# Performance work log

Measured on AMD Instinct MI355X. Metric: run time of the kernel, lower is better.

The kernel has to match this reference:

```python
import jax, jax.numpy as jnp
import numpy as np

N_ENT = 100000


def setup_inputs() -> dict:
    key = jax.random.key(0)
    ks = jax.random.split(key, 10)
    B, D, O, R, E = 50000, 128, 128, 8, 200000
    return {
        "embeddings": jax.random.normal(ks[0], (N_ENT, D), dtype=jnp.float32),
        "head_e": jax.random.normal(ks[1], (B, D), dtype=jnp.float32),
        "tail_e": jax.random.normal(ks[2], (B, D), dtype=jnp.float32),
        "relation_kernel": jax.random.normal(ks[3], (R, D, O), dtype=jnp.float32),
        "self_kernel": jax.random.normal(ks[4], (D, O), dtype=jnp.float32),
        "edge_val": jax.random.uniform(ks[5], (R, E), dtype=jnp.float32),
        "head_idx": jax.random.randint(ks[6], (B,), 0, N_ENT, dtype=jnp.int32),
        "tail_idx": jax.random.randint(ks[7], (B,), 0, N_ENT, dtype=jnp.int32),
        "edge_src": jax.random.randint(ks[8], (R, E), 0, N_ENT, dtype=jnp.int32),
        "edge_dst": jax.random.randint(ks[9], (R, E), 0, N_ENT, dtype=jnp.int32),
    }


def reference(embeddings, head_e, tail_e, relation_kernel, self_kernel,
              edge_val, head_idx, tail_idx, edge_src, edge_dst):
    # Per-relation SpMM: sum_emb[r, row] = sum_{edges e of r with src=row} val[e] * embeddings[dst[e]]
    def spmm(src, dst, val):
        return jax.ops.segment_sum(embeddings[dst] * val[:, None], src,
                                   num_segments=embeddings.shape[0])
    sum_emb = jax.vmap(spmm)(edge_src, edge_dst, edge_val)  # [R, N, D]

    head_update = jnp.take(sum_emb, head_idx, axis=1)  # [R, B, D]
    tail_update = jnp.take(sum_emb, tail_idx, axis=1)  # [R, B, D]

    head_output = head_e @ self_kernel + jnp.einsum('rbd,rdo->bo', head_update, relation_kernel)
    tail_output = tail_e @ self_kernel + jnp.einsum('rbd,rdo->bo', tail_update, relation_kernel)
    return (jax.nn.sigmoid(head_output), jax.nn.sigmoid(tail_output))
```

## Files before the change

### kernel.cpp

```cpp
#include <hip/hip_runtime.h>
#include <hip/hip_bf16.h>
#include <math.h>

#define N_ENT 100000
#define NB    50000
#define NE    200000
#define RR    8
#define NETOT (RR * NE)
#define NSEG  (RR * N_ENT)

typedef float f32x4  __attribute__((ext_vector_type(4)));
typedef short s16x8  __attribute__((ext_vector_type(8)));

__device__ __forceinline__ void split2(float x, short& h, short& l)
{
    unsigned uh = __float_as_uint(x) & 0xffff0000u;
    h = (short)(uh >> 16);
    float r = x - __uint_as_float(uh);
    l = (short)(__float_as_uint(r) >> 16);
}

__global__ __launch_bounds__(256)
void ktconv_k(const float* __restrict__ rel_k, const float* __restrict__ self_k,
              short* __restrict__ Kth, short* __restrict__ Ktl)
{
    const int r = blockIdx.x;
    const float* src = (r < 8) ? rel_k + (size_t)r * 16384 : self_k;
    short* oh = Kth + (size_t)r * 16384;
    short* ol = Ktl + (size_t)r * 16384;
    for (int i = 0; i < 64; ++i) {
        int ix = i * 256 + threadIdx.x;
        int d = ix >> 7, o = ix & 127;
        short h, l;
        split2(src[ix], h, l);
        oh[o * 128 + d] = h;
        ol[o * 128 + d] = l;
    }
}

template<bool FINAL, bool ACCUM>
__global__ __launch_bounds__(256)
void gemm_mfma_k(const float* __restrict__ X, int xstride,
                 const short* __restrict__ Kth, const short* __restrict__ Ktl,
                 int nkc,
                 const float* __restrict__ Abuf, const int* __restrict__ idx,
                 float* __restrict__ out, int nrows)
{
    __shared__ short Bh[128][136];
    __shared__ short Bl[128][136];

    const int t     = threadIdx.x;
    const int wv    = t >> 6;
    const int lane  = t & 63;
    const int col16 = lane & 15;
    const int g     = lane >> 4;
    const int rowbase = blockIdx.x * 128 + wv * 32;

    f32x4 acc[2][8];
#pragma unroll
    for (int m = 0; m < 2; ++m)
#pragma unroll
        for (int c = 0; c < 8; ++c) acc[m][c] = (f32x4){0.f, 0.f, 0.f, 0.f};

    for (int kc = 0; kc < nkc; ++kc) {
        __syncthreads();
        {
            const s16x8* gh = (const s16x8*)(Kth + (size_t)kc * 16384);
            const s16x8* gl = (const s16x8*)(Ktl + (size_t)kc * 16384);
#pragma unroll
            for (int i = 0; i < 8; ++i) {
                int f = t + i * 256;
                int o = f >> 4, c = f & 15;
                *(s16x8*)&Bh[o][c * 8] = gh[f];
                *(s16x8*)&Bl[o][c * 8] = gl[f];
            }
        }
        __syncthreads();

#pragma unroll
        for (int s = 0; s < 4; ++s) {
            s16x8 ah[2], al[2];
#pragma unroll
            for (int m = 0; m < 2; ++m) {
                int r = rowbase + m * 16 + col16;
                if (r > nrows - 1) r = nrows - 1;
                const float* xp = X + (size_t)r * xstride + kc * 128 + s * 32 + g * 8;
                float4 u0 = *(const float4*)xp;
                float4 u1 = *(const float4*)(xp + 4);
                float u[8] = {u0.x, u0.y, u0.z, u0.w, u1.x, u1.y, u1.z, u1.w};
#pragma unroll
                for (int j = 0; j < 8; ++j) {
                    short h, l; split2(u[j], h, l);
                    ah[m][j] = h; al[m][j] = l;
                }
            }
#pragma unroll
            for (int c = 0; c < 8; ++c) {
                s16x8 bh = *(const s16x8*)&Bh[c * 16 + col16][s * 32 + g * 8];
                s16x8 bl = *(const s16x8*)&Bl[c * 16 + col16][s * 32 + g * 8];
#pragma unroll
                for (int m = 0; m < 2; ++m) {
                    acc[m][c] = __builtin_amdgcn_mfma_f32_16x16x32_bf16(ah[m], bh, acc[m][c], 0, 0, 0);
                    acc[m][c] = __builtin_amdgcn_mfma_f32_16x16x32_bf16(ah[m], bl, acc[m][c], 0, 0, 0);
                    acc[m][c] = __builtin_amdgcn_mfma_f32_16x16x32_bf16(al[m], bh, acc[m][c], 0, 0, 0);
                }
            }
        }
    }

#pragma unroll
    for (int m = 0; m < 2; ++m) {
#pragma unroll
        for (int j = 0; j < 4; ++j) {
            int row = rowbase + m * 16 + g * 4 + j;
            if (row >= nrows) continue;
            float* op = out + (size_t)row * 128;
            if (FINAL) {
                int gi = idx[row];
                const float* Ar = Abuf + (size_t)gi * 128;
#pragma unroll
                for (int c = 0; c < 8; ++c) {
                    int col = c * 16 + col16;
                    float x = acc[m][c][j] + Ar[col];
                    op[col] = 1.f / (1.f + __expf(-x));
                }
            } else if (ACCUM) {
#pragma unroll
                for (int c = 0; c < 8; ++c) {
                    int col = c * 16 + col16;
                    op[col] += acc[m][c][j];
                }
            } else {
#pragma unroll
                for (int c = 0; c < 8; ++c)
                    op[c * 16 + col16] = acc[m][c][j];
            }
        }
    }
}

__global__ __launch_bounds__(256)
void count_k(const int* __restrict__ edge_src, unsigned* __restrict__ cnt)
{
    int g = blockIdx.x * 256 + threadIdx.x;
    int r = g / NE;
    int src = edge_src[g];
    atomicAdd(&cnt[r * N_ENT + src], 1u);
}

__global__ __launch_bounds__(256)
void scan1_k(const unsigned* __restrict__ cnt, unsigned* __restrict__ offs,
             unsigned* __restrict__ bsum)
{
    __shared__ unsigned s[256];
    const int t = threadIdx.x;
    const int base = blockIdx.x * 1024;
    unsigned v[4], sum = 0;
#pragma unroll
    for (int i = 0; i < 4; ++i) {
        int ix = base + t * 4 + i;
        v[i] = (ix < NSEG) ? cnt[ix] : 0u;
        sum += v[i];
    }
    s[t] = sum; __syncthreads();
    for (int off = 1; off < 256; off <<= 1) {
        unsigned x = (t >= off) ? s[t - off] : 0u;
        __syncthreads();
        s[t] += x;
        __syncthreads();
    }
    unsigned run = s[t] - sum;
#pragma unroll
    for (int i = 0; i < 4; ++i) {
        int ix = base + t * 4 + i;
        if (ix < NSEG) offs[ix] = run;
        run += v[i];
    }
    if (t == 255) bsum[blockIdx.x] = s[255];
}

__global__ __launch_bounds__(256)
void scan2_k(unsigned* __restrict__ bsum, int nb)
{
    __shared__ unsigned s[256];
    __shared__ unsigned carry;
    const int t = threadIdx.x;
    if (t == 0) carry = 0;
    __syncthreads();
    for (int base = 0; base < nb; base += 256) {
        unsigned v = (base + t < nb) ? bsum[base + t] : 0u;
        s[t] = v; __syncthreads();
        for (int off = 1; off < 256; off <<= 1) {
            unsigned x = (t >= off) ? s[t - off] : 0u;
            __syncthreads();
            s[t] += x;
            __syncthreads();
        }
        unsigned tot = s[255];
        unsigned excl = s[t] - v + carry;
        if (base + t < nb) bsum[base + t] = excl;
        __syncthreads();
        if (t == 0) carry += tot;
        __syncthreads();
    }
}

__global__ __launch_bounds__(256)
void scan3_k(unsigned* __restrict__ offs, const unsigned* __restrict__ bsum)
{
    const int base = blockIdx.x * 1024;
    unsigned add = bsum[blockIdx.x];
#pragma unroll
    for (int i = 0; i < 4; ++i) {
        int ix = base + threadIdx.x * 4 + i;
        if (ix < NSEG) offs[ix] += add;
    }
    if (blockIdx.x == 0 && threadIdx.x == 0) offs[NSEG] = NETOT;
}

__global__ __launch_bounds__(256)
void fill_k(const int* __restrict__ edge_src, const int* __restrict__ edge_dst,
            const float* __restrict__ edge_val,
            const unsigned* __restrict__ offs, unsigned* __restrict__ cursor,
            int2* __restrict__ recs)
{
    int g = blockIdx.x * 256 + threadIdx.x;
    int r = g / NE;
    int src = edge_src[g];
    int seg = r * N_ENT + src;
    unsigned pos = offs[seg] + atomicAdd(&cursor[seg], 1u);
    int2 rec;
    rec.x = edge_dst[g];
    rec.y = __float_as_int(edge_val[g]);
    recs[pos] = rec;
}

__global__ __launch_bounds__(256)
void segsum_k(const unsigned* __restrict__ offs_r, const int2* __restrict__ recs,
              const float* __restrict__ emb, float* __restrict__ B, int nrel)
{
    int wid  = (blockIdx.x * 256 + threadIdx.x) >> 6;
    int lane = threadIdx.x & 63;
    int j = wid / N_ENT;
    int s = wid - j * N_ENT;
    unsigned e0 = offs_r[wid];
    unsigned e1 = offs_r[wid + 1];
    float2 acc = {0.f, 0.f};
    for (unsigned e = e0; e < e1; ++e) {
        int2 rec = recs[e];
        float v = __int_as_float(rec.y);
        float2 y = *(const float2*)(emb + (size_t)rec.x * 128 + lane * 2);
        acc.x = fmaf(v, y.x, acc.x);
        acc.y = fmaf(v, y.y, acc.y);
    }
    *(float2*)(B + ((size_t)s * nrel + j) * 128 + lane * 2) = acc;
}

extern "C" void kernel_launch(void* const* d_in, const int* in_sizes, int n_in,
                              void* d_out, int out_size, void* d_ws, size_t ws_size,
                              hipStream_t stream)
{
    const float* emb      = (const float*)d_in[0];
    const float* head_e   = (const float*)d_in[1];
    const float* tail_e   = (const float*)d_in[2];
    const float* rel_k    = (const float*)d_in[3];
    const float* self_k   = (const float*)d_in[4];
    const float* edge_val = (const float*)d_in[5];
    const int*   head_idx = (const int*)d_in[6];
    const int*   tail_idx = (const int*)d_in[7];
    const int*   edge_src = (const int*)d_in[8];
    const int*   edge_dst = (const int*)d_in[9];
    float* out = (float*)d_out;

    char* p = (char*)d_ws;
    auto take = [&](size_t bytes) -> char* {
        char* q = p; p += (bytes + 255) & ~(size_t)255; return q;
    };
    float*    A    = (float*)take((size_t)N_ENT * 128 * sizeof(float));
    int2*     recs = (int2*)take((size_t)NETOT * sizeof(int2));
    unsigned* cnt  = (unsigned*)take((size_t)NSEG * sizeof(unsigned));
    unsigned* offs = (unsigned*)take(((size_t)NSEG + 1) * sizeof(unsigned));
    unsigned* bsum = (unsigned*)take(1024 * sizeof(unsigned));
    short*    Kth  = (short*)take((size_t)9 * 16384 * sizeof(short));
    short*    Ktl  = (short*)take((size_t)9 * 16384 * sizeof(short));
    float*    Bbuf = (float*)p;

    size_t used    = (size_t)(p - (char*)d_ws);
    size_t avail   = (ws_size > used) ? ws_size - used : 0;
    size_t per_rel = (size_t)N_ENT * 128 * sizeof(float);
    int RPG = (int)(avail / per_rel);
    if (RPG > RR) RPG = RR;
    if (RPG < 1)  RPG = 1;

    const int NB1 = (NSEG + 1023) / 1024;
    dim3 blk(256);

    ktconv_k<<<9, blk, 0, stream>>>(rel_k, self_k, Kth, Ktl);
    hipMemsetAsync(cnt, 0, (size_t)NSEG * sizeof(unsigned), stream);
    count_k<<<NETOT / 256, blk, 0, stream>>>(edge_src, cnt);
    scan1_k<<<NB1, blk, 0, stream>>>(cnt, offs, bsum);
    scan2_k<<<1, blk, 0, stream>>>(bsum, NB1);
    scan3_k<<<NB1, blk, 0, stream>>>(offs, bsum);
    hipMemsetAsync(cnt, 0, (size_t)NSEG * sizeof(unsigned), stream);
    fill_k<<<NETOT / 256, blk, 0, stream>>>(edge_src, edge_dst, edge_val,
                                            offs, cnt, recs);

    const int gy = (N_ENT + 127) / 128;
    int first = 1;
    for (int g0 = 0; g0 < RR; ) {
        int nr = (RR - g0 < RPG) ? RR - g0 : RPG;
        int gs = nr * (N_ENT / 4);
        segsum_k<<<gs, blk, 0, stream>>>(offs + (size_t)g0 * N_ENT, recs,
                                         emb, Bbuf, nr);
        if (first)
            gemm_mfma_k<false, false><<<gy, blk, 0, stream>>>(
                Bbuf, nr * 128,
                Kth + (size_t)g0 * 16384, Ktl + (size_t)g0 * 16384, nr,
                nullptr, nullptr, A, N_ENT);
        else
            gemm_mfma_k<false, true><<<gy, blk, 0, stream>>>(
                Bbuf, nr * 128,
                Kth + (size_t)g0 * 16384, Ktl + (size_t)g0 * 16384, nr,
                nullptr, nullptr, A, N_ENT);
        first = 0;
        g0 += nr;
    }

    const int gb = (NB + 127) / 128;
    gemm_mfma_k<true, false><<<gb, blk, 0, stream>>>(
        head_e, 128, Kth + (size_t)8 * 16384, Ktl + (size_t)8 * 16384, 1,
        A, head_idx, out, NB);
    gemm_mfma_k<true, false><<<gb, blk, 0, stream>>>(
        tail_e, 128, Kth + (size_t)8 * 16384, Ktl + (size_t)8 * 16384, 1,
        A, tail_idx, out + (size_t)NB * 128, NB);
}
```

Baseline: 700.0 us.

## Batch segment-sum over relations per wave with prefetched edge gathers

```diff
diff --git a/kernel.cpp b/kernel.cpp
--- a/kernel.cpp
+++ b/kernel.cpp
@@ -235,25 +235,79 @@
     recs[pos] = rec;
 }
 
+template<int NR>
 __global__ __launch_bounds__(256)
 void segsum_k(const unsigned* __restrict__ offs_r, const int2* __restrict__ recs,
-              const float* __restrict__ emb, float* __restrict__ B, int nrel)
-{
-    int wid  = (blockIdx.x * 256 + threadIdx.x) >> 6;
-    int lane = threadIdx.x & 63;
-    int j = wid / N_ENT;
-    int s = wid - j * N_ENT;
-    unsigned e0 = offs_r[wid];
-    unsigned e1 = offs_r[wid + 1];
-    float2 acc = {0.f, 0.f};
-    for (unsigned e = e0; e < e1; ++e) {
-        int2 rec = recs[e];
-        float v = __int_as_float(rec.y);
-        float2 y = *(const float2*)(emb + (size_t)rec.x * 128 + lane * 2);
-        acc.x = fmaf(v, y.x, acc.x);
-        acc.y = fmaf(v, y.y, acc.y);
-    }
-    *(float2*)(B + ((size_t)s * nrel + j) * 128 + lane * 2) = acc;
+              const float* __restrict__ emb, float* __restrict__ B)
+{
+    constexpr int T = 4;
+    const int s    = (blockIdx.x * 256 + threadIdx.x) >> 6;
+    const int lane = threadIdx.x & 63;
+    if (s >= N_ENT) return;
+
+    unsigned e0[NR]; int n[NR];
+#pragma unroll
+    for (int j = 0; j < NR; ++j) {
+        unsigned a = offs_r[(size_t)j * N_ENT + s];
+        unsigned b = offs_r[(size_t)j * N_ENT + s + 1];
+        e0[j] = a; n[j] = (int)(b - a);
+    }
+
+    int2 rec[NR][T];
+#pragma unroll
+    for (int j = 0; j < NR; ++j)
+#pragma unroll
+        for (int i = 0; i < T; ++i)
+            if (i < n[j]) rec[j][i] = recs[e0[j] + i];
+
+    float2 y[NR][T];
+#pragma unroll
+    for (int j = 0; j < NR; ++j)
+#pragma unroll
+        for (int i = 0; i < T; ++i)
+            if (i < n[j])
+                y[j][i] = *(const float2*)(emb + (size_t)rec[j][i].x * 128 + lane * 2);
+
+    float2 acc[NR];
+#pragma unroll
+    for (int j = 0; j < NR; ++j) acc[j] = (float2){0.f, 0.f};
+#pragma unroll
+    for (int j = 0; j < NR; ++j)
+#pragma unroll
+        for (int i = 0; i < T; ++i)
+            if (i < n[j]) {
+                float v = __int_as_float(rec[j][i].y);
+                acc[j].x = fmaf(v, y[j][i].x, acc[j].x);
+                acc[j].y = fmaf(v, y[j][i].y, acc[j].y);
+            }
+
+#pragma unroll
+    for (int j = 0; j < NR; ++j) {
+        for (int i = T; i < n[j]; ++i) {
+            int2 rc = recs[e0[j] + i];
+            float v = __int_as_float(rc.y);
+            float2 yy = *(const float2*)(emb + (size_t)rc.x * 128 + lane * 2);
+            acc[j].x = fmaf(v, yy.x, acc[j].x);
+            acc[j].y = fmaf(v, yy.y, acc[j].y);
+        }
+    }
+
+#pragma unroll
+    for (int j = 0; j < NR; ++j)
+        *(float2*)(B + ((size_t)s * NR + j) * 128 + lane * 2) = acc[j];
+}
+
+static void launch_segsum(int nr, const unsigned* offs_r, const int2* recs,
+                          const float* emb, float* B, hipStream_t stream)
+{
+    dim3 blk(256);
+    const int blocks = (N_ENT * 64) / 256;
+    switch (nr) {
+    case 1: segsum_k<1><<<blocks, blk, 0, stream>>>(offs_r, recs, emb, B); break;
+    case 2: segsum_k<2><<<blocks, blk, 0, stream>>>(offs_r, recs, emb, B); break;
+    case 3: segsum_k<3><<<blocks, blk, 0, stream>>>(offs_r, recs, emb, B); break;
+    default: segsum_k<4><<<blocks, blk, 0, stream>>>(offs_r, recs, emb, B); break;
+    }
 }
 
 extern "C" void kernel_launch(void* const* d_in, const int* in_sizes, int n_in,
@@ -289,8 +343,8 @@
     size_t avail   = (ws_size > used) ? ws_size - used : 0;
     size_t per_rel = (size_t)N_ENT * 128 * sizeof(float);
     int RPG = (int)(avail / per_rel);
-    if (RPG > RR) RPG = RR;
-    if (RPG < 1)  RPG = 1;
+    if (RPG > 4) RPG = 4;
+    if (RPG < 1) RPG = 1;
 
     const int NB1 = (NSEG + 1023) / 1024;
     dim3 blk(256);
@@ -309,9 +363,7 @@
     int first = 1;
     for (int g0 = 0; g0 < RR; ) {
         int nr = (RR - g0 < RPG) ? RR - g0 : RPG;
-        int gs = nr * (N_ENT / 4);
-        segsum_k<<<gs, blk, 0, stream>>>(offs + (size_t)g0 * N_ENT, recs,
-                                         emb, Bbuf, nr);
+        launch_segsum(nr, offs + (size_t)g0 * N_ENT, recs, emb, Bbuf, stream);
         if (first)
             gemm_mfma_k<false, false><<<gy, blk, 0, stream>>>(
                 Bbuf, nr * 128,
```

Result: no change. 688.9 us (-1.6%).
